# Performance work log

Measured on AMD Instinct MI355X. Metric: run time of the kernel, lower is better.

Reference implementation:

```python
import jax, jax.numpy as jnp
import numpy as np

BETA = 0.1
TRUNC = 1.0
MIN_VALID_RATIO = 0.3


def _wls_affine(x, y, w):
    # Weighted least squares fit of y ~ s*x + t over the last axis.
    sw = w.sum(-1)
    swx = (w * x).sum(-1)
    swy = (w * y).sum(-1)
    swxx = (w * x * x).sum(-1)
    swxy = (w * x * y).sum(-1)
    det = sw * swxx - swx * swx
    det = jnp.where(jnp.abs(det) < 1e-12, 1e-12, det)
    s = (sw * swxy - swx * swy) / det
    t = (swxx * swy - swx * swxy) / det
    return s, t


def _align_depth_affine(x, y, w, trunc):
    # Truncated robust affine alignment: initial WLS fit, then refit with
    # weights of points whose weighted residual exceeds `trunc` zeroed out
    # (falling back to the original weights if everything is truncated).
    s0, t0 = _wls_affine(x, y, w)
    e = w * jnp.abs(s0[..., None] * x + t0[..., None] - y)
    w2 = w * (e < trunc).astype(w.dtype)
    w2 = jnp.where(w2.sum(-1, keepdims=True) > 1e-8, w2, w)
    return _wls_affine(x, y, w2)


def _smooth(err, beta):
    if beta == 0:
        return err
    return jnp.where(err < beta, 0.5 * err * err / beta, err - 0.5 * beta)


def setup_inputs() -> dict:
    key = jax.random.key(0)
    k1, k2, k3 = jax.random.split(key, 3)
    B = 8
    P = 4096  # num_patches
    K = 256   # patch_pixel_count
    N = P * K
    pred_depth = jax.random.uniform(k1, (B, N), jnp.float32, 0.05, 5.0)
    gt_depth = jax.random.uniform(k2, (B, N), jnp.float32, 0.05, 5.0)
    mask = jax.random.bernoulli(k3, 0.8, (B, N))
    global_scale = jnp.ones((B,), jnp.float32)
    return {
        "pred_depth": pred_depth,
        "gt_depth": gt_depth,
        "mask": mask,
        "global_scale": global_scale,
        "num_patches": P,
        "patch_pixel_count": K,
    }


def reference(pred_depth, gt_depth, mask, global_scale, num_patches, patch_pixel_count):
    B = pred_depth.shape[0]
    P, K = num_patches, patch_pixel_count
    x = pred_depth.reshape(B, P, K)
    y = gt_depth.reshape(B, P, K)
    m = mask.reshape(B, P, K).astype(x.dtype)

    valid_ratio = m.mean(-1)                      # (B, P)
    msum = m.sum(-1)
    mean_depth = jnp.where(msum > 0, (y * m).sum(-1) / jnp.maximum(msum, 1.0), 1.0)

    w = m / jnp.maximum(y, 1e-5)                  # alignment weights (B, P, K)
    s, t = _align_depth_affine(x, y, w, TRUNC)    # (B, P) scale / shift per patch

    ratio = s / jnp.maximum(global_scale[:, None], 1e-12)
    gs_ok = jnp.where(global_scale[:, None] > 0, (ratio >= 0.1) & (ratio <= 10.0), True)
    valid = (valid_ratio >= MIN_VALID_RATIO) & (s > 0) & gs_ok  # (B, P)

    aligned = s[..., None] * x + t[..., None]
    pw = m / jnp.maximum(y, 0.1 * mean_depth[..., None])
    patch_loss = _smooth(jnp.abs(aligned - y) * pw, BETA).mean(-1)  # (B, P)

    vf = valid.astype(x.dtype)
    cnt = vf.sum()
    loss = jnp.where(cnt > 0, (patch_loss * vf).sum() / jnp.maximum(cnt, 1.0), 0.0)
    return loss
```

## Files before the change

### kernel.cpp

```cpp
#include <hip/hip_runtime.h>


#define WPB 4
#define NSLOTS 64
#define MAXBLK 2048

__device__ __forceinline__ float wred(float v) {
  #pragma unroll
  for (int off = 32; off; off >>= 1) v += __shfl_xor(v, off, 64);
  return v;
}

__device__ __forceinline__ float frcp(float x) {
  return __builtin_amdgcn_rcpf(x);
}

__global__ __launch_bounds__(256) void moge_patch_kernel(
    const float* __restrict__ xg,
    const float* __restrict__ yg,
    const int*   __restrict__ mg,
    const float* __restrict__ gsg,
    const int*   __restrict__ pP,
    const int*   __restrict__ pK,
    int B,
    float* __restrict__ ws,
    float* __restrict__ out) {
  const int P = pP[0];
  const int K = pK[0];
  const int lane = threadIdx.x & 63;
  const int wib  = threadIdx.x >> 6;
  const int total_patches = B * P;
  const int wave_stride = gridDim.x * WPB;
  const float invK = 1.0f / (float)K;
  const bool fast = (K == 256);

  for (int patch = blockIdx.x * WPB + wib; patch < total_patches;
       patch += wave_stride) {
    const long base = (long)patch * (long)K;
    const float* xp = xg + base;
    const float* yp = yg + base;
    const int*   mp = mg + base;

    float xr[4], yr[4], mr[4], wr[4];

    float sw = 0.f, swx = 0.f, swy = 0.f, swxx = 0.f, swxy = 0.f;
    float msum = 0.f, symsum = 0.f;
    if (fast) {
      const float4 x4 = *(const float4*)(xp + lane * 4);
      const float4 y4 = *(const float4*)(yp + lane * 4);
      const int4   m4 = *(const int4*)(mp + lane * 4);
      xr[0] = x4.x; xr[1] = x4.y; xr[2] = x4.z; xr[3] = x4.w;
      yr[0] = y4.x; yr[1] = y4.y; yr[2] = y4.z; yr[3] = y4.w;
      mr[0] = m4.x ? 1.f : 0.f; mr[1] = m4.y ? 1.f : 0.f;
      mr[2] = m4.z ? 1.f : 0.f; mr[3] = m4.w ? 1.f : 0.f;
      #pragma unroll
      for (int i = 0; i < 4; ++i) {
        const float m = mr[i], xx = xr[i], yy = yr[i];
        const float w = m * frcp(fmaxf(yy, 1e-5f));
        wr[i] = w;
        const float wx = w * xx;
        sw += w; swx += wx; swy = fmaf(w, yy, swy);
        swxx = fmaf(wx, xx, swxx); swxy = fmaf(wx, yy, swxy);
        msum += m; symsum = fmaf(m, yy, symsum);
      }
    } else {
      for (int j = lane; j < K; j += 64) {
        const float m = mp[j] ? 1.f : 0.f;
        const float xx = xp[j], yy = yp[j];
        const float w = m * frcp(fmaxf(yy, 1e-5f));
        const float wx = w * xx;
        sw += w; swx += wx; swy = fmaf(w, yy, swy);
        swxx = fmaf(wx, xx, swxx); swxy = fmaf(wx, yy, swxy);
        msum += m; symsum = fmaf(m, yy, symsum);
      }
    }
    sw = wred(sw); swx = wred(swx); swy = wred(swy);
    swxx = wred(swxx); swxy = wred(swxy);
    msum = wred(msum); symsum = wred(symsum);

    float det = sw * swxx - swx * swx;
    if (fabsf(det) < 1e-12f) det = 1e-12f;
    float rdet = frcp(det);
    const float s0 = (sw * swxy - swx * swy) * rdet;
    const float t0 = (swxx * swy - swx * swxy) * rdet;

    float sw2 = 0.f, swx2 = 0.f, swy2 = 0.f, swxx2 = 0.f, swxy2 = 0.f;
    if (fast) {
      #pragma unroll
      for (int i = 0; i < 4; ++i) {
        const float xx = xr[i], yy = yr[i], w = wr[i];
        const float e = w * fabsf(fmaf(s0, xx, t0) - yy);
        const float w2 = (e < 1.0f) ? w : 0.f;
        const float w2x = w2 * xx;
        sw2 += w2; swx2 += w2x; swy2 = fmaf(w2, yy, swy2);
        swxx2 = fmaf(w2x, xx, swxx2); swxy2 = fmaf(w2x, yy, swxy2);
      }
    } else {
      for (int j = lane; j < K; j += 64) {
        const float m = mp[j] ? 1.f : 0.f;
        const float xx = xp[j], yy = yp[j];
        const float w = m * frcp(fmaxf(yy, 1e-5f));
        const float e = w * fabsf(fmaf(s0, xx, t0) - yy);
        const float w2 = (e < 1.0f) ? w : 0.f;
        const float w2x = w2 * xx;
        sw2 += w2; swx2 += w2x; swy2 = fmaf(w2, yy, swy2);
        swxx2 = fmaf(w2x, xx, swxx2); swxy2 = fmaf(w2x, yy, swxy2);
      }
    }
    sw2 = wred(sw2); swx2 = wred(swx2); swy2 = wred(swy2);
    swxx2 = wred(swxx2); swxy2 = wred(swxy2);

    if (sw2 > 1e-8f) {
      sw = sw2; swx = swx2; swy = swy2; swxx = swxx2; swxy = swxy2;
    }
    det = sw * swxx - swx * swx;
    if (fabsf(det) < 1e-12f) det = 1e-12f;
    rdet = frcp(det);
    const float s = (sw * swxy - swx * swy) * rdet;
    const float t = (swxx * swy - swx * swxy) * rdet;

    const float mean_depth =
        (msum > 0.f) ? (symsum * frcp(fmaxf(msum, 1.f))) : 1.f;
    const float yfloor = 0.1f * mean_depth;

    float lsum = 0.f;
    if (fast) {
      #pragma unroll
      for (int i = 0; i < 4; ++i) {
        const float xx = xr[i], yy = yr[i], m = mr[i];
        const float pw = m * frcp(fmaxf(yy, yfloor));
        const float err = fabsf(fmaf(s, xx, t) - yy) * pw;
        lsum += (err < 0.1f) ? (5.0f * err * err) : (err - 0.05f);
      }
    } else {
      for (int j = lane; j < K; j += 64) {
        const float m = mp[j] ? 1.f : 0.f;
        const float xx = xp[j], yy = yp[j];
        const float pw = m * frcp(fmaxf(yy, yfloor));
        const float err = fabsf(fmaf(s, xx, t) - yy) * pw;
        lsum += (err < 0.1f) ? (5.0f * err * err) : (err - 0.05f);
      }
    }
    lsum = wred(lsum);
    const float patch_loss = lsum * invK;

    const float gs = gsg[patch / P];
    const float ratio = s * frcp(fmaxf(gs, 1e-12f));
    const bool gs_ok = (gs > 0.f) ? (ratio >= 0.1f && ratio <= 10.0f) : true;
    const bool valid = (msum * invK >= 0.3f) && (s > 0.f) && gs_ok;

    if (lane == 0 && valid) {
      const int slot = patch & (NSLOTS - 1);
      atomicAdd(&ws[slot], patch_loss);
      atomicAdd(&ws[NSLOTS + slot], 1.0f);
    }
  }

  __syncthreads();
  __shared__ int is_last;
  if (threadIdx.x == 0) {
    unsigned int old = atomicAdd((unsigned int*)(ws + 2 * NSLOTS), 1u);
    is_last = (old == gridDim.x - 1) ? 1 : 0;
  }
  __syncthreads();
  if (is_last && threadIdx.x < 64) {
    __builtin_amdgcn_fence(__ATOMIC_ACQUIRE, "agent");
    float l = __hip_atomic_load(&ws[threadIdx.x], __ATOMIC_RELAXED,
                                __HIP_MEMORY_SCOPE_AGENT);
    float c = __hip_atomic_load(&ws[NSLOTS + threadIdx.x], __ATOMIC_RELAXED,
                                __HIP_MEMORY_SCOPE_AGENT);
    l = wred(l);
    c = wred(c);
    if (threadIdx.x == 0) out[0] = (c > 0.f) ? (l / fmaxf(c, 1.f)) : 0.f;
  }
}

extern "C" void kernel_launch(void* const* d_in, const int* in_sizes, int n_in,
                              void* d_out, int out_size, void* d_ws, size_t ws_size,
                              hipStream_t stream) {
  const float* pred = (const float*)d_in[0];
  const float* gt   = (const float*)d_in[1];
  const int*   mask = (const int*)d_in[2];
  const float* gs   = (const float*)d_in[3];
  const int*   pP   = (const int*)d_in[4];
  const int*   pK   = (const int*)d_in[5];
  const int B = in_sizes[3];
  const long total_pixels = (long)in_sizes[0];
  float* ws = (float*)d_ws;

  hipMemsetAsync(ws, 0, (2 * NSLOTS + 1) * sizeof(float), stream);

  long est_patches = total_pixels / 256;
  long blocks = (est_patches + WPB - 1) / WPB;
  if (blocks < 1) blocks = 1;
  if (blocks > MAXBLK) blocks = MAXBLK;
  moge_patch_kernel<<<(int)blocks, 256, 0, stream>>>(pred, gt, mask, gs, pP,
                                                     pK, B, ws, (float*)d_out);
}
```

Baseline: 146.4 us.

## Prefetch next patch in persistent loop and use DPP wave reductions

The K==256 path is restructured as a software-pipelined persistent loop. Each wave loads the next patch's x, y and mask while it computes the current one, so memory latency overlaps with the three reduction passes. All wave reductions switch from shfl_xor butterflies to DPP row shifts and row broadcasts, finishing with a readlane of lane 63. This cuts LDS-based shuffle latency, at the cost of extra registers for the prefetched data and a redundant load on the last iteration.

New measurement: 144.1 us. No clear change (-1.6%).

```diff
diff --git a/kernel.cpp b/kernel.cpp
--- a/kernel.cpp
+++ b/kernel.cpp
@@ -5,10 +5,18 @@
 #define NSLOTS 64
 #define MAXBLK 2048
 
-__device__ __forceinline__ float wred(float v) {
-  #pragma unroll
-  for (int off = 32; off; off >>= 1) v += __shfl_xor(v, off, 64);
-  return v;
+__device__ __forceinline__ float wredu(float v) {
+#define DPP_ADD(ctrl)                                                        \
+  v += __int_as_float(__builtin_amdgcn_update_dpp(                           \
+      0, __float_as_int(v), (ctrl), 0xf, 0xf, true))
+  DPP_ADD(0x111);
+  DPP_ADD(0x112);
+  DPP_ADD(0x114);
+  DPP_ADD(0x118);
+  DPP_ADD(0x142);
+  DPP_ADD(0x143);
+#undef DPP_ADD
+  return __int_as_float(__builtin_amdgcn_readlane(__float_as_int(v), 63));
 }
 
 __device__ __forceinline__ float frcp(float x) {
@@ -32,38 +40,112 @@
   const int total_patches = B * P;
   const int wave_stride = gridDim.x * WPB;
   const float invK = 1.0f / (float)K;
-  const bool fast = (K == 256);
-
-  for (int patch = blockIdx.x * WPB + wib; patch < total_patches;
-       patch += wave_stride) {
-    const long base = (long)patch * (long)K;
-    const float* xp = xg + base;
-    const float* yp = yg + base;
-    const int*   mp = mg + base;
-
-    float xr[4], yr[4], mr[4], wr[4];
-
-    float sw = 0.f, swx = 0.f, swy = 0.f, swxx = 0.f, swxy = 0.f;
-    float msum = 0.f, symsum = 0.f;
-    if (fast) {
-      const float4 x4 = *(const float4*)(xp + lane * 4);
-      const float4 y4 = *(const float4*)(yp + lane * 4);
-      const int4   m4 = *(const int4*)(mp + lane * 4);
-      xr[0] = x4.x; xr[1] = x4.y; xr[2] = x4.z; xr[3] = x4.w;
-      yr[0] = y4.x; yr[1] = y4.y; yr[2] = y4.z; yr[3] = y4.w;
-      mr[0] = m4.x ? 1.f : 0.f; mr[1] = m4.y ? 1.f : 0.f;
-      mr[2] = m4.z ? 1.f : 0.f; mr[3] = m4.w ? 1.f : 0.f;
-      #pragma unroll
-      for (int i = 0; i < 4; ++i) {
-        const float m = mr[i], xx = xr[i], yy = yr[i];
-        const float w = m * frcp(fmaxf(yy, 1e-5f));
-        wr[i] = w;
-        const float wx = w * xx;
-        sw += w; swx += wx; swy = fmaf(w, yy, swy);
-        swxx = fmaf(wx, xx, swxx); swxy = fmaf(wx, yy, swxy);
-        msum += m; symsum = fmaf(m, yy, symsum);
-      }
-    } else {
+
+  if (K == 256) {
+    int patch = blockIdx.x * WPB + wib;
+    if (patch < total_patches) {
+      const int loff = lane * 4;
+      long base = (long)patch * 256 + loff;
+      float4 x4 = *(const float4*)(xg + base);
+      float4 y4 = *(const float4*)(yg + base);
+      int4   m4 = *(const int4*)(mg + base);
+
+      for (;;) {
+        const int next = patch + wave_stride;
+        const bool has_next = next < total_patches;
+        const long nbase = (has_next ? (long)next * 256 : 0) + loff;
+        const float4 nx4 = *(const float4*)(xg + nbase);
+        const float4 ny4 = *(const float4*)(yg + nbase);
+        const int4   nm4 = *(const int4*)(mg + nbase);
+
+        float xr[4] = {x4.x, x4.y, x4.z, x4.w};
+        float yr[4] = {y4.x, y4.y, y4.z, y4.w};
+        float mr[4] = {m4.x ? 1.f : 0.f, m4.y ? 1.f : 0.f,
+                       m4.z ? 1.f : 0.f, m4.w ? 1.f : 0.f};
+        float wr[4];
+
+        float sw = 0.f, swx = 0.f, swy = 0.f, swxx = 0.f, swxy = 0.f;
+        float msum = 0.f, symsum = 0.f;
+        #pragma unroll
+        for (int i = 0; i < 4; ++i) {
+          const float m = mr[i], xx = xr[i], yy = yr[i];
+          const float w = m * frcp(fmaxf(yy, 1e-5f));
+          wr[i] = w;
+          const float wx = w * xx;
+          sw += w; swx += wx; swy = fmaf(w, yy, swy);
+          swxx = fmaf(wx, xx, swxx); swxy = fmaf(wx, yy, swxy);
+          msum += m; symsum = fmaf(m, yy, symsum);
+        }
+        sw = wredu(sw); swx = wredu(swx); swy = wredu(swy);
+        swxx = wredu(swxx); swxy = wredu(swxy);
+
+        float det = sw * swxx - swx * swx;
+        if (fabsf(det) < 1e-12f) det = 1e-12f;
+        float rdet = frcp(det);
+        const float s0 = (sw * swxy - swx * swy) * rdet;
+        const float t0 = (swxx * swy - swx * swxy) * rdet;
+
+        float sw2 = 0.f, swx2 = 0.f, swy2 = 0.f, swxx2 = 0.f, swxy2 = 0.f;
+        #pragma unroll
+        for (int i = 0; i < 4; ++i) {
+          const float xx = xr[i], yy = yr[i], w = wr[i];
+          const float e = w * fabsf(fmaf(s0, xx, t0) - yy);
+          const float w2 = (e < 1.0f) ? w : 0.f;
+          const float w2x = w2 * xx;
+          sw2 += w2; swx2 += w2x; swy2 = fmaf(w2, yy, swy2);
+          swxx2 = fmaf(w2x, xx, swxx2); swxy2 = fmaf(w2x, yy, swxy2);
+        }
+        sw2 = wredu(sw2); swx2 = wredu(swx2); swy2 = wredu(swy2);
+        swxx2 = wredu(swxx2); swxy2 = wredu(swxy2);
+        msum = wredu(msum); symsum = wredu(symsum);
+
+        if (sw2 > 1e-8f) {
+          sw = sw2; swx = swx2; swy = swy2; swxx = swxx2; swxy = swxy2;
+        }
+        det = sw * swxx - swx * swx;
+        if (fabsf(det) < 1e-12f) det = 1e-12f;
+        rdet = frcp(det);
+        const float s = (sw * swxy - swx * swy) * rdet;
+        const float t = (swxx * swy - swx * swxy) * rdet;
+
+        const float mean_depth =
+            (msum > 0.f) ? (symsum * frcp(fmaxf(msum, 1.f))) : 1.f;
+        const float yfloor = 0.1f * mean_depth;
+
+        float lsum = 0.f;
+        #pragma unroll
+        for (int i = 0; i < 4; ++i) {
+          const float pw = mr[i] * frcp(fmaxf(yr[i], yfloor));
+          const float err = fabsf(fmaf(s, xr[i], t) - yr[i]) * pw;
+          lsum += (err < 0.1f) ? (5.0f * err * err) : (err - 0.05f);
+        }
+        const float patch_loss = wredu(lsum) * invK;
+
+        const float gs = gsg[patch / P];
+        const float ratio = s * frcp(fmaxf(gs, 1e-12f));
+        const bool gs_ok = (gs > 0.f) ? (ratio >= 0.1f && ratio <= 10.0f) : true;
+        const bool valid = (msum * invK >= 0.3f) && (s > 0.f) && gs_ok;
+
+        if (lane == 0 && valid) {
+          const int slot = patch & (NSLOTS - 1);
+          atomicAdd(&ws[slot], patch_loss);
+          atomicAdd(&ws[NSLOTS + slot], 1.0f);
+        }
+
+        if (!has_next) break;
+        patch = next; x4 = nx4; y4 = ny4; m4 = nm4;
+      }
+    }
+  } else {
+    for (int patch = blockIdx.x * WPB + wib; patch < total_patches;
+         patch += wave_stride) {
+      const long base = (long)patch * (long)K;
+      const float* xp = xg + base;
+      const float* yp = yg + base;
+      const int*   mp = mg + base;
+
+      float sw = 0.f, swx = 0.f, swy = 0.f, swxx = 0.f, swxy = 0.f;
+      float msum = 0.f, symsum = 0.f;
       for (int j = lane; j < K; j += 64) {
         const float m = mp[j] ? 1.f : 0.f;
         const float xx = xp[j], yy = yp[j];
@@ -73,29 +155,17 @@
         swxx = fmaf(wx, xx, swxx); swxy = fmaf(wx, yy, swxy);
         msum += m; symsum = fmaf(m, yy, symsum);
       }
-    }
-    sw = wred(sw); swx = wred(swx); swy = wred(swy);
-    swxx = wred(swxx); swxy = wred(swxy);
-    msum = wred(msum); symsum = wred(symsum);
-
-    float det = sw * swxx - swx * swx;
-    if (fabsf(det) < 1e-12f) det = 1e-12f;
-    float rdet = frcp(det);
-    const float s0 = (sw * swxy - swx * swy) * rdet;
-    const float t0 = (swxx * swy - swx * swxy) * rdet;
-
-    float sw2 = 0.f, swx2 = 0.f, swy2 = 0.f, swxx2 = 0.f, swxy2 = 0.f;
-    if (fast) {
-      #pragma unroll
-      for (int i = 0; i < 4; ++i) {
-        const float xx = xr[i], yy = yr[i], w = wr[i];
-        const float e = w * fabsf(fmaf(s0, xx, t0) - yy);
-        const float w2 = (e < 1.0f) ? w : 0.f;
-        const float w2x = w2 * xx;
-        sw2 += w2; swx2 += w2x; swy2 = fmaf(w2, yy, swy2);
-        swxx2 = fmaf(w2x, xx, swxx2); swxy2 = fmaf(w2x, yy, swxy2);
-      }
-    } else {
+      sw = wredu(sw); swx = wredu(swx); swy = wredu(swy);
+      swxx = wredu(swxx); swxy = wredu(swxy);
+      msum = wredu(msum); symsum = wredu(symsum);
+
+      float det = sw * swxx - swx * swx;
+      if (fabsf(det) < 1e-12f) det = 1e-12f;
+      float rdet = frcp(det);
+      const float s0 = (sw * swxy - swx * swy) * rdet;
+      const float t0 = (swxx * swy - swx * swxy) * rdet;
+
+      float sw2 = 0.f, swx2 = 0.f, swy2 = 0.f, swxx2 = 0.f, swxy2 = 0.f;
       for (int j = lane; j < K; j += 64) {
         const float m = mp[j] ? 1.f : 0.f;
         const float xx = xp[j], yy = yp[j];
@@ -106,33 +176,23 @@
         sw2 += w2; swx2 += w2x; swy2 = fmaf(w2, yy, swy2);
         swxx2 = fmaf(w2x, xx, swxx2); swxy2 = fmaf(w2x, yy, swxy2);
       }
-    }
-    sw2 = wred(sw2); swx2 = wred(swx2); swy2 = wred(swy2);
-    swxx2 = wred(swxx2); swxy2 = wred(swxy2);
-
-    if (sw2 > 1e-8f) {
-      sw = sw2; swx = swx2; swy = swy2; swxx = swxx2; swxy = swxy2;
-    }
-    det = sw * swxx - swx * swx;
-    if (fabsf(det) < 1e-12f) det = 1e-12f;
-    rdet = frcp(det);
-    const float s = (sw * swxy - swx * swy) * rdet;
-    const float t = (swxx * swy - swx * swxy) * rdet;
-
-    const float mean_depth =
-        (msum > 0.f) ? (symsum * frcp(fmaxf(msum, 1.f))) : 1.f;
-    const float yfloor = 0.1f * mean_depth;
-
-    float lsum = 0.f;
-    if (fast) {
-      #pragma unroll
-      for (int i = 0; i < 4; ++i) {
-        const float xx = xr[i], yy = yr[i], m = mr[i];
-        const float pw = m * frcp(fmaxf(yy, yfloor));
-        const float err = fabsf(fmaf(s, xx, t) - yy) * pw;
-        lsum += (err < 0.1f) ? (5.0f * err * err) : (err - 0.05f);
-      }
-    } else {
+      sw2 = wredu(sw2); swx2 = wredu(swx2); swy2 = wredu(swy2);
+      swxx2 = wredu(swxx2); swxy2 = wredu(swxy2);
+
+      if (sw2 > 1e-8f) {
+        sw = sw2; swx = swx2; swy = swy2; swxx = swxx2; swxy = swxy2;
+      }
+      det = sw * swxx - swx * swx;
+      if (fabsf(det) < 1e-12f) det = 1e-12f;
+      rdet = frcp(det);
+      const float s = (sw * swxy - swx * swy) * rdet;
+      const float t = (swxx * swy - swx * swxy) * rdet;
+
+      const float mean_depth =
+          (msum > 0.f) ? (symsum * frcp(fmaxf(msum, 1.f))) : 1.f;
+      const float yfloor = 0.1f * mean_depth;
+
+      float lsum = 0.f;
       for (int j = lane; j < K; j += 64) {
         const float m = mp[j] ? 1.f : 0.f;
         const float xx = xp[j], yy = yp[j];
@@ -140,19 +200,18 @@
         const float err = fabsf(fmaf(s, xx, t) - yy) * pw;
         lsum += (err < 0.1f) ? (5.0f * err * err) : (err - 0.05f);
       }
-    }
-    lsum = wred(lsum);
-    const float patch_loss = lsum * invK;
-
-    const float gs = gsg[patch / P];
-    const float ratio = s * frcp(fmaxf(gs, 1e-12f));
-    const bool gs_ok = (gs > 0.f) ? (ratio >= 0.1f && ratio <= 10.0f) : true;
-    const bool valid = (msum * invK >= 0.3f) && (s > 0.f) && gs_ok;
-
-    if (lane == 0 && valid) {
-      const int slot = patch & (NSLOTS - 1);
-      atomicAdd(&ws[slot], patch_loss);
-      atomicAdd(&ws[NSLOTS + slot], 1.0f);
+      const float patch_loss = wredu(lsum) * invK;
+
+      const float gs = gsg[patch / P];
+      const float ratio = s * frcp(fmaxf(gs, 1e-12f));
+      const bool gs_ok = (gs > 0.f) ? (ratio >= 0.1f && ratio <= 10.0f) : true;
+      const bool valid = (msum * invK >= 0.3f) && (s > 0.f) && gs_ok;
+
+      if (lane == 0 && valid) {
+        const int slot = patch & (NSLOTS - 1);
+        atomicAdd(&ws[slot], patch_loss);
+        atomicAdd(&ws[NSLOTS + slot], 1.0f);
+      }
     }
   }
 
@@ -169,8 +228,8 @@
                                 __HIP_MEMORY_SCOPE_AGENT);
     float c = __hip_atomic_load(&ws[NSLOTS + threadIdx.x], __ATOMIC_RELAXED,
                                 __HIP_MEMORY_SCOPE_AGENT);
-    l = wred(l);
-    c = wred(c);
+    l = wredu(l);
+    c = wredu(c);
     if (threadIdx.x == 0) out[0] = (c > 0.f) ? (l / fmaxf(c, 1.f)) : 0.f;
   }
 }
```
